# Optimization experiments

Hardware: AMD Instinct MI355X
Metric: run time of the kernel (lower is better)

The kernel has to match this reference:

```python
import jax, jax.numpy as jnp
import numpy as np

KH, KW = 3, 3
STRIDE = (1, 1)
PADDING = (1, 1)
DILATION = (1, 1)


def setup_inputs() -> dict:
    key = jax.random.key(0)
    k1, k2, k3, k4, k5 = jax.random.split(key, 5)
    B, Cin, H, W = 8, 64, 128, 128
    Cout = 64
    Ho, Wo = 128, 128  # stride 1, pad 1, k=3 -> same spatial size
    K = KH * KW
    return {
        "input": jax.random.normal(k1, (B, Cin, H, W), dtype=jnp.float32),
        "offset": jax.random.normal(k2, (B, 2 * K, Ho, Wo), dtype=jnp.float32),
        "mask": jax.random.uniform(k3, (B, K, Ho, Wo), dtype=jnp.float32),
        "weight": jax.random.normal(k4, (Cout, Cin, KH, KW), dtype=jnp.float32) * 0.05,
        "bias": jax.random.normal(k5, (Cout,), dtype=jnp.float32) * 0.05,
    }


def _deform_conv2d(x, weight, offset, mask, bias, stride, padding, dilation):
    B, Cin, H, W = x.shape
    Cout, Cing, kh, kw = weight.shape
    G = Cin // Cing                      # weight groups
    K = kh * kw
    Goff = offset.shape[1] // (2 * K)    # offset groups
    Ho, Wo = offset.shape[2], offset.shape[3]
    Cg = Cin // Goff                     # channels per offset group
    sh, sw = stride
    ph, pw = padding
    dh, dw = dilation

    # offsets laid out as (y, x) pairs per kernel tap per offset group
    off = offset.reshape(B, Goff, K, 2, Ho, Wo)
    ky = (jnp.arange(K) // kw).astype(jnp.float32) * dh   # [K]
    kx = (jnp.arange(K) % kw).astype(jnp.float32) * dw
    gy = (jnp.arange(Ho).astype(jnp.float32) * sh - ph)    # [Ho]
    gx = (jnp.arange(Wo).astype(jnp.float32) * sw - pw)
    # sampling positions: [B, Goff, K, Ho, Wo]
    py = off[:, :, :, 0] + ky[None, None, :, None, None] + gy[None, None, None, :, None]
    px = off[:, :, :, 1] + kx[None, None, :, None, None] + gx[None, None, None, None, :]

    y0 = jnp.floor(py)
    x0 = jnp.floor(px)
    ly = py - y0
    lx = px - x0
    y0i = y0.astype(jnp.int32)
    x0i = x0.astype(jnp.int32)

    x_g = x.reshape(B, Goff, Cg, H * W)

    def gather(yi, xi):
        # zero padding outside the image
        valid = (yi >= 0) & (yi < H) & (xi >= 0) & (xi < W)
        yc = jnp.clip(yi, 0, H - 1)
        xc = jnp.clip(xi, 0, W - 1)
        idx = (yc * W + xc).reshape(B, Goff, K * Ho * Wo)
        v = jnp.take_along_axis(x_g, idx[:, :, None, :], axis=3)  # [B,Goff,Cg,K*Ho*Wo]
        return v * valid.reshape(B, Goff, 1, K * Ho * Wo)

    w00 = ((1 - ly) * (1 - lx)).reshape(B, Goff, 1, K * Ho * Wo)
    w01 = ((1 - ly) * lx).reshape(B, Goff, 1, K * Ho * Wo)
    w10 = (ly * (1 - lx)).reshape(B, Goff, 1, K * Ho * Wo)
    w11 = (ly * lx).reshape(B, Goff, 1, K * Ho * Wo)

    sampled = w00 * gather(y0i, x0i)
    sampled = sampled + w01 * gather(y0i, x0i + 1)
    sampled = sampled + w10 * gather(y0i + 1, x0i)
    sampled = sampled + w11 * gather(y0i + 1, x0i + 1)
    sampled = sampled.reshape(B, Goff, Cg, K, Ho, Wo)

    if mask is not None:
        sampled = sampled * mask.reshape(B, Goff, 1, K, Ho, Wo)

    # grouped conv accumulate
    sampled = sampled.reshape(B, G, Cing, K, Ho, Wo)
    w = weight.reshape(G, Cout // G, Cing, K)
    out = jnp.einsum('gock,bgcksq->bgosq', w, sampled).reshape(B, Cout, Ho, Wo)
    if bias is not None:
        out = out + bias[None, :, None, None]
    return out


def reference(input, offset, mask, weight, bias):
    return _deform_conv2d(input, weight, offset, mask, bias, STRIDE, PADDING, DILATION)
```

## Files before the change

kernel.cpp:

```cpp
#include <hip/hip_runtime.h>

#define HH 128
#define WW 128
#define HW (HH*WW)
#define XT_BYTES ((size_t)8 * HW * 64 * 2)
#define WT_BYTES ((size_t)9 * 2 * 4 * 64 * 8 * 2)

typedef __attribute__((ext_vector_type(8))) short short8;
typedef __attribute__((ext_vector_type(4))) float f32x4;

static __device__ __forceinline__ unsigned short f2bf(float f) {
    unsigned int u = __float_as_uint(f);
    u += 0x7fffu + ((u >> 16) & 1u);
    return (unsigned short)(u >> 16);
}
static __device__ __forceinline__ float bf2f(unsigned short h) {
    return __uint_as_float((unsigned int)h << 16);
}

__global__ void wtrans_kernel(const float* __restrict__ w, unsigned short* __restrict__ wt) {
    int i = blockIdx.x * 256 + threadIdx.x;
    if (i < 9 * 2 * 4 * 64 * 8) {
        int e  = i & 7;
        int l  = (i >> 3) & 63;
        int wv = (i >> 9) & 3;
        int kf = (i >> 11) & 1;
        int k  = i >> 12;
        int co = wv * 16 + (l & 15);
        int c  = kf * 32 + (l >> 4) * 8 + e;
        wt[i] = f2bf(w[(co * 64 + c) * 9 + k]);
    }
}

__global__ __launch_bounds__(256) void xtrans_kernel(const float* __restrict__ x,
                                                     unsigned int* __restrict__ xt32) {
    __shared__ float tile[64][65];
    const int bid = blockIdx.x;
    const int b   = bid >> 8;
    const int hw0 = (bid & 255) << 6;
    const int t   = threadIdx.x;
    #pragma unroll
    for (int i = 0; i < 16; ++i) {
        int idx = (i << 8) + t;
        int c = idx >> 6, j = idx & 63;
        tile[c][j] = x[(size_t)(((b << 6) + c) << 14) + hw0 + j];
    }
    __syncthreads();
    #pragma unroll
    for (int i = 0; i < 8; ++i) {
        int idx = (i << 8) + t;
        int cp = idx & 31, hw = idx >> 5;
        unsigned u = (unsigned)f2bf(tile[2 * cp][hw]) | ((unsigned)f2bf(tile[2 * cp + 1][hw]) << 16);
        xt32[((size_t)((b << 14) + hw0 + hw) << 5) + cp] = u;
    }
}

__global__ __launch_bounds__(256, 4) void deform_nhwc(
    const unsigned short* __restrict__ xt,
    const float* __restrict__ off,
    const float* __restrict__ msk,
    const unsigned short* __restrict__ wt,
    const float* __restrict__ bias,
    float* __restrict__ out)
{
    __shared__ __align__(16) unsigned short s_tile[2][64][72];
    __shared__ __align__(16) unsigned char meta_mem[18432];
    float4* mwS = (float4*)meta_mem;
    int4*   moS = (int4*)(meta_mem + 9216);
    float*  out_t = (float*)meta_mem;

    const int t   = threadIdx.x;
    const int bid = blockIdx.x;
    const int b   = bid & 7;
    const int rem = bid >> 3;
    const int ho  = rem >> 1;
    const int wo0 = (rem & 1) << 6;
    const int l   = t & 63;
    const int wv_id = __builtin_amdgcn_readfirstlane(t >> 6);

    short8 wtf[2][2];
    #pragma unroll
    for (int kf = 0; kf < 2; ++kf)
        wtf[0][kf] = *(const short8*)(wt + (((kf * 4 + wv_id) * 64 + l) << 3));

    for (int i = t; i < 9 * 64; i += 256) {
        int p = i & 63;
        int k = i >> 6;
        int wo = wo0 + p;
        int obase = ((b * 18 + 2 * k) * HH + ho) * WW + wo;
        float oy = off[obase];
        float ox = off[obase + HW];
        float m  = msk[((b * 9 + k) * HH + ho) * WW + wo];
        float py = oy + (float)(k / 3) + (float)(ho - 1);
        float px = ox + (float)(k % 3) + (float)(wo - 1);
        float fy = floorf(py), fx = floorf(px);
        float ly = py - fy,    lx = px - fx;
        int y0 = (int)fy, x0 = (int)fx;
        int y1 = y0 + 1,  x1 = x0 + 1;
        float vy0 = (y0 >= 0 && y0 < HH) ? 1.f : 0.f;
        float vy1 = (y1 >= 0 && y1 < HH) ? 1.f : 0.f;
        float vx0 = (x0 >= 0 && x0 < WW) ? 1.f : 0.f;
        float vx1 = (x1 >= 0 && x1 < WW) ? 1.f : 0.f;
        float w00 = (1.f - ly) * (1.f - lx) * m * vy0 * vx0;
        float w01 = (1.f - ly) * lx         * m * vy0 * vx1;
        float w10 = ly         * (1.f - lx) * m * vy1 * vx0;
        float w11 = ly         * lx         * m * vy1 * vx1;
        int yc0 = min(max(y0, 0), HH - 1), yc1 = min(max(y1, 0), HH - 1);
        int xc0 = min(max(x0, 0), WW - 1), xc1 = min(max(x1, 0), WW - 1);
        mwS[i] = make_float4(w00, w01, w10, w11);
        moS[i] = make_int4((yc0 * WW + xc0) << 7, (yc0 * WW + xc1) << 7,
                           (yc1 * WW + xc0) << 7, (yc1 * WW + xc1) << 7);
    }

    const char* ib = (const char*)xt + (size_t)b * HW * 128;
    const int ch0 = (l & 7) << 3;
    const int ch2 = ch0 << 1;

    __syncthreads();

    auto sample_tap = [&](int k, int bb) {
        #pragma unroll
        for (int r = 0; r < 2; ++r) {
            int px = (wv_id << 4) + (r << 3) + (l >> 3);
            int4   ob = moS[k * 64 + px];
            float4 ww = mwS[k * 64 + px];
            short8 c00 = *(const short8*)(ib + ob.x + ch2);
            short8 c01 = *(const short8*)(ib + ob.y + ch2);
            short8 c10 = *(const short8*)(ib + ob.z + ch2);
            short8 c11 = *(const short8*)(ib + ob.w + ch2);
            unsigned u[4];
            #pragma unroll
            for (int e = 0; e < 8; e += 2) {
                float v0 = ww.x * bf2f((unsigned short)c00[e])   + ww.y * bf2f((unsigned short)c01[e])
                         + ww.z * bf2f((unsigned short)c10[e])   + ww.w * bf2f((unsigned short)c11[e]);
                float v1 = ww.x * bf2f((unsigned short)c00[e+1]) + ww.y * bf2f((unsigned short)c01[e+1])
                         + ww.z * bf2f((unsigned short)c10[e+1]) + ww.w * bf2f((unsigned short)c11[e+1]);
                u[e >> 1] = (unsigned)f2bf(v0) | ((unsigned)f2bf(v1) << 16);
            }
            uint4 uv = make_uint4(u[0], u[1], u[2], u[3]);
            *(uint4*)&s_tile[bb][px][ch0] = uv;
        }
    };

    sample_tap(0, 0);
    __syncthreads();

    f32x4 acc[4];
    #pragma unroll
    for (int g = 0; g < 4; ++g) acc[g] = (f32x4){0.f, 0.f, 0.f, 0.f};

    #pragma unroll
    for (int s = 0; s < 9; ++s) {
        if (s < 8) {
            const int kn = s + 1;
            #pragma unroll
            for (int kf = 0; kf < 2; ++kf)
                wtf[kn & 1][kf] = *(const short8*)(wt + ((((kn * 2 + kf) * 4 + wv_id) * 64 + l) << 3));
            sample_tap(kn, kn & 1);
        }
        #pragma unroll
        for (int g = 0; g < 4; ++g) {
            const int prow = g * 16 + (l & 15);
            const unsigned short* rp = &s_tile[s & 1][prow][(l >> 4) * 8];
            union { short8 v; unsigned long long q[2]; } ua0, ua1;
            ua0.q[0] = *(const unsigned long long*)(rp);
            ua0.q[1] = *(const unsigned long long*)(rp + 4);
            ua1.q[0] = *(const unsigned long long*)(rp + 32);
            ua1.q[1] = *(const unsigned long long*)(rp + 36);
            acc[g] = __builtin_amdgcn_mfma_f32_16x16x32_bf16(ua0.v, wtf[s & 1][0], acc[g], 0, 0, 0);
            acc[g] = __builtin_amdgcn_mfma_f32_16x16x32_bf16(ua1.v, wtf[s & 1][1], acc[g], 0, 0, 0);
        }
        __syncthreads();
    }

    const int cb = wv_id << 4;
    const float bv = bias[cb + (l & 15)];
    #pragma unroll
    for (int g = 0; g < 4; ++g) {
        int co = cb + (l & 15);
        int pxb = g * 16 + (l >> 4) * 4;
        #pragma unroll
        for (int r = 0; r < 4; ++r)
            out_t[co * 68 + pxb + r] = acc[g][r] + bv;
    }
    __syncthreads();
    float* outb = out + (size_t)b * 64 * HW + (size_t)ho * WW + wo0;
    #pragma unroll
    for (int j = 0; j < 4; ++j) {
        int co  = (t >> 4) + j * 16;
        int px0 = (t & 15) << 2;
        float4 v = *(float4*)&out_t[co * 68 + px0];
        *(float4*)&outb[(size_t)co * HW + px0] = v;
    }
}

__global__ __launch_bounds__(256, 4) void deform_fallback(
    const float* __restrict__ x, const float* __restrict__ off,
    const float* __restrict__ msk, const float* __restrict__ wraw,
    const float* __restrict__ bias, float* __restrict__ out)
{
    __shared__ unsigned short s_tile[2][64][68];
    __shared__ __align__(16) unsigned char meta_mem[18432];
    float4* mwS = (float4*)meta_mem;
    int4*   moS = (int4*)(meta_mem + 9216);
    float*  out_t = (float*)meta_mem;

    const int t   = threadIdx.x;
    const int bid = blockIdx.x;
    const int b   = bid & 7;
    const int rem = bid >> 3;
    const int ho  = rem >> 1;
    const int wo0 = (rem & 1) << 6;
    const int l   = t & 63;
    const int wv_id = __builtin_amdgcn_readfirstlane(t >> 6);
    const int c0  = wv_id << 4;
    const int cb  = wv_id << 4;

    short8 wtf[2][2];
    #pragma unroll
    for (int kf = 0; kf < 2; ++kf) {
        short8 f;
        int co = cb + (l & 15);
        int cbase = kf * 32 + (l >> 4) * 8;
        #pragma unroll
        for (int e = 0; e < 8; ++e) f[e] = (short)f2bf(wraw[(co * 64 + cbase + e) * 9 + 0]);
        wtf[0][kf] = f;
    }

    for (int i = t; i < 9 * 64; i += 256) {
        int p = i & 63;
        int k = i >> 6;
        int wo = wo0 + p;
        int obase = ((b * 18 + 2 * k) * HH + ho) * WW + wo;
        float oy = off[obase];
        float ox = off[obase + HW];
        float m  = msk[((b * 9 + k) * HH + ho) * WW + wo];
        float py = oy + (float)(k / 3) + (float)(ho - 1);
        float px = ox + (float)(k % 3) + (float)(wo - 1);
        float fy = floorf(py), fx = floorf(px);
        float ly = py - fy,    lx = px - fx;
        int y0 = (int)fy, x0 = (int)fx;
        int y1 = y0 + 1,  x1 = x0 + 1;
        float vy0 = (y0 >= 0 && y0 < HH) ? 1.f : 0.f;
        float vy1 = (y1 >= 0 && y1 < HH) ? 1.f : 0.f;
        float vx0 = (x0 >= 0 && x0 < WW) ? 1.f : 0.f;
        float vx1 = (x1 >= 0 && x1 < WW) ? 1.f : 0.f;
        float w00 = (1.f - ly) * (1.f - lx) * m * vy0 * vx0;
        float w01 = (1.f - ly) * lx         * m * vy0 * vx1;
        float w10 = ly         * (1.f - lx) * m * vy1 * vx0;
        float w11 = ly         * lx         * m * vy1 * vx1;
        int yc0 = min(max(y0, 0), HH - 1), yc1 = min(max(y1, 0), HH - 1);
        int xc0 = min(max(x0, 0), WW - 1), xc1 = min(max(x1, 0), WW - 1);
        mwS[i] = make_float4(w00, w01, w10, w11);
        moS[i] = make_int4(yc0 * WW + xc0, yc0 * WW + xc1,
                           yc1 * WW + xc0, yc1 * WW + xc1);
    }

    const int p = t & 63;
    const float* xb = x + (size_t)(b * 64 + c0) * HW;
    __syncthreads();

    {
        float4 wv = mwS[p];
        int4   ov = moS[p];
        const float* pc = xb;
        #pragma unroll
        for (int i = 0; i < 16; i += 4) {
            float v0 = wv.x * pc[ov.x] + wv.y * pc[ov.y] + wv.z * pc[ov.z] + wv.w * pc[ov.w]; pc += HW;
            float v1 = wv.x * pc[ov.x] + wv.y * pc[ov.y] + wv.z * pc[ov.z] + wv.w * pc[ov.w]; pc += HW;
            float v2 = wv.x * pc[ov.x] + wv.y * pc[ov.y] + wv.z * pc[ov.z] + wv.w * pc[ov.w]; pc += HW;
            float v3 = wv.x * pc[ov.x] + wv.y * pc[ov.y] + wv.z * pc[ov.z] + wv.w * pc[ov.w]; pc += HW;
            uint2 u;
            u.x = (unsigned)f2bf(v0) | ((unsigned)f2bf(v1) << 16);
            u.y = (unsigned)f2bf(v2) | ((unsigned)f2bf(v3) << 16);
            *(uint2*)&s_tile[0][p][c0 + i] = u;
        }
    }
    __syncthreads();

    f32x4 acc[4];
    #pragma unroll
    for (int g = 0; g < 4; ++g) acc[g] = (f32x4){0.f, 0.f, 0.f, 0.f};

    #pragma unroll
    for (int s = 0; s < 9; ++s) {
        if (s < 8) {
            const int kn = s + 1;
            #pragma unroll
            for (int kf = 0; kf < 2; ++kf) {
                short8 f;
                int co = cb + (l & 15);
                int cbase = kf * 32 + (l >> 4) * 8;
                #pragma unroll
                for (int e = 0; e < 8; ++e) f[e] = (short)f2bf(wraw[(co * 64 + cbase + e) * 9 + kn]);
                wtf[kn & 1][kf] = f;
            }
            float4 wv = mwS[kn * 64 + p];
            int4   ov = moS[kn * 64 + p];
            const float* pc = xb;
            #pragma unroll
            for (int i = 0; i < 16; i += 4) {
                float v0 = wv.x * pc[ov.x] + wv.y * pc[ov.y] + wv.z * pc[ov.z] + wv.w * pc[ov.w]; pc += HW;
                float v1 = wv.x * pc[ov.x] + wv.y * pc[ov.y] + wv.z * pc[ov.z] + wv.w * pc[ov.w]; pc += HW;
                float v2 = wv.x * pc[ov.x] + wv.y * pc[ov.y] + wv.z * pc[ov.z] + wv.w * pc[ov.w]; pc += HW;
                float v3 = wv.x * pc[ov.x] + wv.y * pc[ov.y] + wv.z * pc[ov.z] + wv.w * pc[ov.w]; pc += HW;
                uint2 u;
                u.x = (unsigned)f2bf(v0) | ((unsigned)f2bf(v1) << 16);
                u.y = (unsigned)f2bf(v2) | ((unsigned)f2bf(v3) << 16);
                *(uint2*)&s_tile[kn & 1][p][c0 + i] = u;
            }
        }
        #pragma unroll
        for (int g = 0; g < 4; ++g) {
            const int prow = g * 16 + (l & 15);
            const unsigned short* rp = &s_tile[s & 1][prow][(l >> 4) * 8];
            union { short8 v; unsigned long long q[2]; } ua0, ua1;
            ua0.q[0] = *(const unsigned long long*)(rp);
            ua0.q[1] = *(const unsigned long long*)(rp + 4);
            ua1.q[0] = *(const unsigned long long*)(rp + 32);
            ua1.q[1] = *(const unsigned long long*)(rp + 36);
            acc[g] = __builtin_amdgcn_mfma_f32_16x16x32_bf16(ua0.v, wtf[s & 1][0], acc[g], 0, 0, 0);
            acc[g] = __builtin_amdgcn_mfma_f32_16x16x32_bf16(ua1.v, wtf[s & 1][1], acc[g], 0, 0, 0);
        }
        __syncthreads();
    }

    const float bv = bias[cb + (l & 15)];
    #pragma unroll
    for (int g = 0; g < 4; ++g) {
        int co = cb + (l & 15);
        int pxb = g * 16 + (l >> 4) * 4;
        #pragma unroll
        for (int r = 0; r < 4; ++r)
            out_t[co * 68 + pxb + r] = acc[g][r] + bv;
    }
    __syncthreads();
    float* outb = out + (size_t)b * 64 * HW + (size_t)ho * WW + wo0;
    #pragma unroll
    for (int j = 0; j < 4; ++j) {
        int co  = (t >> 4) + j * 16;
        int px0 = (t & 15) << 2;
        float4 v = *(float4*)&out_t[co * 68 + px0];
        *(float4*)&outb[(size_t)co * HW + px0] = v;
    }
}

extern "C" void kernel_launch(void* const* d_in, const int* in_sizes, int n_in,
                              void* d_out, int out_size, void* d_ws, size_t ws_size,
                              hipStream_t stream) {
    const float* x    = (const float*)d_in[0];
    const float* off  = (const float*)d_in[1];
    const float* msk  = (const float*)d_in[2];
    const float* w    = (const float*)d_in[3];
    const float* bias = (const float*)d_in[4];
    float* out = (float*)d_out;

    const size_t need = XT_BYTES + WT_BYTES;
    if (d_ws != nullptr && ws_size >= need) {
        unsigned int*   xt32 = (unsigned int*)d_ws;
        unsigned short* wt   = (unsigned short*)((char*)d_ws + XT_BYTES);
        xtrans_kernel<<<2048, 256, 0, stream>>>(x, xt32);
        wtrans_kernel<<<144, 256, 0, stream>>>(w, wt);
        deform_nhwc<<<2048, 256, 0, stream>>>((const unsigned short*)xt32, off, msk, wt, bias, out);
    } else {
        deform_fallback<<<2048, 256, 0, stream>>>(x, off, msk, w, bias, out);
    }
}
```

Measured before the change: 54.13 us.

## Shrink LDS with XOR-swizzled tiles and fp16 bilinear weights, raise occupancy

```diff
diff --git a/kernel.cpp b/kernel.cpp
--- a/kernel.cpp
+++ b/kernel.cpp
@@ -1,4 +1,5 @@
 #include <hip/hip_runtime.h>
+#include <hip/hip_fp16.h>
 
 #define HH 128
 #define WW 128
@@ -16,6 +17,12 @@
 }
 static __device__ __forceinline__ float bf2f(unsigned short h) {
     return __uint_as_float((unsigned int)h << 16);
+}
+static __device__ __forceinline__ float blo(unsigned int u) {
+    return __uint_as_float(u << 16);
+}
+static __device__ __forceinline__ float bhi(unsigned int u) {
+    return __uint_as_float(u & 0xffff0000u);
 }
 
 __global__ void wtrans_kernel(const float* __restrict__ w, unsigned short* __restrict__ wt) {
@@ -55,7 +62,7 @@
     }
 }
 
-__global__ __launch_bounds__(256, 4) void deform_nhwc(
+__global__ __launch_bounds__(256, 5) void deform_nhwc(
     const unsigned short* __restrict__ xt,
     const float* __restrict__ off,
     const float* __restrict__ msk,
@@ -63,11 +70,9 @@
     const float* __restrict__ bias,
     float* __restrict__ out)
 {
-    __shared__ __align__(16) unsigned short s_tile[2][64][72];
-    __shared__ __align__(16) unsigned char meta_mem[18432];
-    float4* mwS = (float4*)meta_mem;
-    int4*   moS = (int4*)(meta_mem + 9216);
-    float*  out_t = (float*)meta_mem;
+    __shared__ __align__(16) unsigned char smem[30208];
+    int4*  moS = (int4*)(smem + 16384);
+    uint2* mwH = (uint2*)(smem + 25600);
 
     const int t   = threadIdx.x;
     const int bid = blockIdx.x;
@@ -107,42 +112,52 @@
         float w11 = ly         * lx         * m * vy1 * vx1;
         int yc0 = min(max(y0, 0), HH - 1), yc1 = min(max(y1, 0), HH - 1);
         int xc0 = min(max(x0, 0), WW - 1), xc1 = min(max(x1, 0), WW - 1);
-        mwS[i] = make_float4(w00, w01, w10, w11);
         moS[i] = make_int4((yc0 * WW + xc0) << 7, (yc0 * WW + xc1) << 7,
                            (yc1 * WW + xc0) << 7, (yc1 * WW + xc1) << 7);
+        __half2 hA = __floats2half2_rn(w00, w01);
+        __half2 hB = __floats2half2_rn(w10, w11);
+        mwH[i] = make_uint2(*(unsigned int*)&hA, *(unsigned int*)&hB);
     }
 
     const char* ib = (const char*)xt + (size_t)b * HW * 128;
-    const int ch0 = (l & 7) << 3;
-    const int ch2 = ch0 << 1;
-
-    __syncthreads();
-
-    auto sample_tap = [&](int k, int bb) {
+    const int chb  = (l & 7) << 4;
+    const int px0_ = (wv_id << 4) + (l >> 3);
+    int st_woff[2];
+    st_woff[0] = px0_ * 128 + (chb ^ ((px0_ & 7) << 4));
+    st_woff[1] = st_woff[0] + 8 * 128;
+    const int lq = (l >> 4) << 4;
+    const int sw = (l & 7) << 4;
+
+    __syncthreads();
+
+    auto sample_tap = [&](int k, unsigned char* dst) {
         #pragma unroll
         for (int r = 0; r < 2; ++r) {
-            int px = (wv_id << 4) + (r << 3) + (l >> 3);
+            const int px = px0_ + (r << 3);
             int4   ob = moS[k * 64 + px];
-            float4 ww = mwS[k * 64 + px];
-            short8 c00 = *(const short8*)(ib + ob.x + ch2);
-            short8 c01 = *(const short8*)(ib + ob.y + ch2);
-            short8 c10 = *(const short8*)(ib + ob.z + ch2);
-            short8 c11 = *(const short8*)(ib + ob.w + ch2);
-            unsigned u[4];
-            #pragma unroll
-            for (int e = 0; e < 8; e += 2) {
-                float v0 = ww.x * bf2f((unsigned short)c00[e])   + ww.y * bf2f((unsigned short)c01[e])
-                         + ww.z * bf2f((unsigned short)c10[e])   + ww.w * bf2f((unsigned short)c11[e]);
-                float v1 = ww.x * bf2f((unsigned short)c00[e+1]) + ww.y * bf2f((unsigned short)c01[e+1])
-                         + ww.z * bf2f((unsigned short)c10[e+1]) + ww.w * bf2f((unsigned short)c11[e+1]);
-                u[e >> 1] = (unsigned)f2bf(v0) | ((unsigned)f2bf(v1) << 16);
-            }
-            uint4 uv = make_uint4(u[0], u[1], u[2], u[3]);
-            *(uint4*)&s_tile[bb][px][ch0] = uv;
+            uint2  wp = mwH[k * 64 + px];
+            float2 wA = __half22float2(*(const __half2*)&wp.x);
+            float2 wB = __half22float2(*(const __half2*)&wp.y);
+            uint4 c00 = *(const uint4*)(ib + (ob.x + chb));
+            uint4 c01 = *(const uint4*)(ib + (ob.y + chb));
+            uint4 c10 = *(const uint4*)(ib + (ob.z + chb));
+            uint4 c11 = *(const uint4*)(ib + (ob.w + chb));
+            uint4 uv;
+            #define CMB(dst_, a0, a1, a2, a3) {                                         \
+                float vlo = wA.x*blo(a0) + wA.y*blo(a1) + wB.x*blo(a2) + wB.y*blo(a3);  \
+                float vhi = wA.x*bhi(a0) + wA.y*bhi(a1) + wB.x*bhi(a2) + wB.y*bhi(a3);  \
+                dst_ = __builtin_amdgcn_perm(__float_as_uint(vhi) + 0x8000u,            \
+                                             __float_as_uint(vlo) + 0x8000u, 0x07060302u); }
+            CMB(uv.x, c00.x, c01.x, c10.x, c11.x);
+            CMB(uv.y, c00.y, c01.y, c10.y, c11.y);
+            CMB(uv.z, c00.z, c01.z, c10.z, c11.z);
+            CMB(uv.w, c00.w, c01.w, c10.w, c11.w);
+            #undef CMB
+            *(uint4*)(dst + st_woff[r]) = uv;
         }
     };
 
-    sample_tap(0, 0);
+    sample_tap(0, smem);
     __syncthreads();
 
     f32x4 acc[4];
@@ -156,41 +171,38 @@
             #pragma unroll
             for (int kf = 0; kf < 2; ++kf)
                 wtf[kn & 1][kf] = *(const short8*)(wt + ((((kn * 2 + kf) * 4 + wv_id) * 64 + l) << 3));
-            sample_tap(kn, kn & 1);
-        }
+            sample_tap(kn, smem + ((kn & 1) << 13));
+        }
+        const unsigned char* rb = smem + ((s & 1) << 13);
         #pragma unroll
         for (int g = 0; g < 4; ++g) {
             const int prow = g * 16 + (l & 15);
-            const unsigned short* rp = &s_tile[s & 1][prow][(l >> 4) * 8];
-            union { short8 v; unsigned long long q[2]; } ua0, ua1;
-            ua0.q[0] = *(const unsigned long long*)(rp);
-            ua0.q[1] = *(const unsigned long long*)(rp + 4);
-            ua1.q[0] = *(const unsigned long long*)(rp + 32);
-            ua1.q[1] = *(const unsigned long long*)(rp + 36);
-            acc[g] = __builtin_amdgcn_mfma_f32_16x16x32_bf16(ua0.v, wtf[s & 1][0], acc[g], 0, 0, 0);
-            acc[g] = __builtin_amdgcn_mfma_f32_16x16x32_bf16(ua1.v, wtf[s & 1][1], acc[g], 0, 0, 0);
+            short8 a0 = *(const short8*)(rb + prow * 128 + (lq ^ sw));
+            short8 a1 = *(const short8*)(rb + prow * 128 + ((64 + lq) ^ sw));
+            acc[g] = __builtin_amdgcn_mfma_f32_16x16x32_bf16(a0, wtf[s & 1][0], acc[g], 0, 0, 0);
+            acc[g] = __builtin_amdgcn_mfma_f32_16x16x32_bf16(a1, wtf[s & 1][1], acc[g], 0, 0, 0);
         }
         __syncthreads();
     }
 
-    const int cb = wv_id << 4;
-    const float bv = bias[cb + (l & 15)];
+    float* out_t = (float*)smem;
+    const int co_e = (wv_id << 4) + (l & 15);
+    const float bv = bias[co_e];
+    const int swE = (co_e & 15) << 4;
     #pragma unroll
     for (int g = 0; g < 4; ++g) {
-        int co = cb + (l & 15);
-        int pxb = g * 16 + (l >> 4) * 4;
-        #pragma unroll
-        for (int r = 0; r < 4; ++r)
-            out_t[co * 68 + pxb + r] = acc[g][r] + bv;
+        int pxb = (g << 6) + ((l >> 4) << 4);
+        float4 v = make_float4(acc[g][0] + bv, acc[g][1] + bv, acc[g][2] + bv, acc[g][3] + bv);
+        *(float4*)((unsigned char*)out_t + co_e * 256 + (pxb ^ swE)) = v;
     }
     __syncthreads();
     float* outb = out + (size_t)b * 64 * HW + (size_t)ho * WW + wo0;
     #pragma unroll
     for (int j = 0; j < 4; ++j) {
-        int co  = (t >> 4) + j * 16;
-        int px0 = (t & 15) << 2;
-        float4 v = *(float4*)&out_t[co * 68 + px0];
-        *(float4*)&outb[(size_t)co * HW + px0] = v;
+        int co   = (t >> 4) + (j << 4);
+        int colb = (t & 15) << 4;
+        float4 v = *(const float4*)((const unsigned char*)out_t + co * 256 + (colb ^ ((co & 15) << 4)));
+        *(float4*)&outb[(size_t)co * HW + ((t & 15) << 2)] = v;
     }
 }
 
```

Measured after the change: 52.73 us. -2.6%, faster.
